# Kernel optimization log

Measured on AMD Instinct MI355X. Metric: run time of the kernel, lower is better.

Reference implementation:

```python
import jax, jax.numpy as jnp
import numpy as np

N_CAMP = 50
DAYS = 365          # execution_duration
N_STATES = 3
BASIS = 1e-10


def setup_inputs() -> dict:
    key = jax.random.key(0)
    k1, k2, k3, k4, k5 = jax.random.split(key, 5)
    adstock = jax.random.uniform(k1, (4096, N_CAMP, DAYS + 1), dtype=jnp.float32)
    mu = jax.random.normal(k2, (3,), dtype=jnp.float32)
    beta = jax.random.normal(k3, (3 * N_CAMP,), dtype=jnp.float32)
    init_prob = jax.random.normal(k4, (1,), dtype=jnp.float32)
    click_prob = jax.random.normal(k5, (1,), dtype=jnp.float32)
    return {"adstock": adstock, "mu": mu, "beta": beta,
            "init_prob": init_prob, "click_prob": click_prob}


def make_transition_matrix(mu, beta, adstock, basis=BASIS):
    b = adstock.shape[0]
    # [N_camp, 4]: zero column + reshaped betas
    beta_r = jnp.concatenate(
        [jnp.zeros((N_CAMP, 1), adstock.dtype), beta.reshape(N_CAMP, 3)], axis=1)
    # tensordot over campaign axis: [b, days, 4]
    O_beta = jnp.einsum('bcd,ck->bdk', adstock[:, :, 1:], beta_r)
    # [-inf, mu0, mu1, mu2]; exp(-inf)=0 kills the (0,0) slot exactly as in TF
    mu_full = jnp.concatenate([jnp.full((1,), -jnp.inf, dtype=mu.dtype), mu])
    mp = (mu_full[None, None, :] + O_beta).reshape(b, DAYS, N_STATES - 1, -1)
    num = jnp.exp(mp)                      # [b, D, 2, 2]
    den = 1.0 + jnp.sum(num, axis=3)       # [b, D, 2]
    main_diag = jnp.concatenate(
        [1.0 / den, jnp.ones((b, DAYS, 1), den.dtype)], axis=-1)   # [b, D, 3]
    lower_diag = jnp.concatenate(
        [num[:, :, 1:, 0] / den[:, :, 1:],
         jnp.zeros((b, DAYS, 1), den.dtype)], axis=-1)             # [b, D, 2]
    upper_diag = num[:, :, :, 1] / den                              # [b, D, 2]
    Q = jnp.zeros((b, DAYS, N_STATES, N_STATES), den.dtype)
    i = jnp.arange(N_STATES)
    Q = Q.at[..., i, i].set(main_diag)                 # main diagonal
    Q = Q.at[..., i[1:], i[:-1]].set(lower_diag)       # k = -1
    Q = Q.at[..., i[:-1], i[1:]].set(upper_diag)       # k = +1
    return jnp.maximum(Q, basis)


def reference(adstock, mu, beta, init_prob, click_prob):
    Q = make_transition_matrix(mu, beta, adstock)
    return Q, jax.nn.sigmoid(init_prob), jax.nn.sigmoid(click_prob)
```

## Files before the change

### kernel.cpp

```cpp
#include <hip/hip_runtime.h>

#define N_CAMP 50
#define DAYS   365
#define BASIS  1e-10f
#define BATCH  4096
#define NTHR   384

__global__ __launch_bounds__(NTHR)
void transition_prob_kernel(const float* __restrict__ adstock,
                            const float* __restrict__ mu,
                            const float* __restrict__ beta,
                            float* __restrict__ out)
{
    __shared__ float sb0[N_CAMP];
    __shared__ float sb1[N_CAMP];
    __shared__ float sb2[N_CAMP];
    __shared__ float smu[3];
    __shared__ float sQ[DAYS * 9];

    const int tid = threadIdx.x;
    const int b   = blockIdx.x;

    if (tid < 3 * N_CAMP) {
        const int c = tid / 3;
        const int k = tid % 3;
        const float v = beta[tid];
        if (k == 0) sb0[c] = v;
        else if (k == 1) sb1[c] = v;
        else sb2[c] = v;
    }
    if (tid < 3) smu[tid] = mu[tid];
    __syncthreads();

    const int d = tid;
    if (d < DAYS) {
        const float* arow = adstock + (size_t)b * (N_CAMP * (DAYS + 1)) + (d + 1);

        float o1 = 0.f, o2 = 0.f, o3 = 0.f;
#pragma unroll 10
        for (int c = 0; c < N_CAMP; ++c) {
            const float a = arow[(size_t)c * (DAYS + 1)];
            o1 = fmaf(a, sb0[c], o1);
            o2 = fmaf(a, sb1[c], o2);
            o3 = fmaf(a, sb2[c], o3);
        }

        const float e1 = expf(smu[0] + o1);
        const float e2 = expf(smu[1] + o2);
        const float e3 = expf(smu[2] + o3);
        const float inv0 = 1.0f / (1.0f + e1);
        const float inv1 = 1.0f / (1.0f + e2 + e3);

        float* q = &sQ[d * 9];
        q[0] = fmaxf(inv0,      BASIS);
        q[1] = fmaxf(e1 * inv0, BASIS);
        q[2] = BASIS;
        q[3] = fmaxf(e2 * inv1, BASIS);
        q[4] = fmaxf(inv1,      BASIS);
        q[5] = fmaxf(e3 * inv1, BASIS);
        q[6] = BASIS;
        q[7] = BASIS;
        q[8] = 1.0f;
    }
    __syncthreads();

    float* dst = out + (size_t)b * (DAYS * 9);
#pragma unroll
    for (int i = tid; i < DAYS * 9; i += NTHR) {
        dst[i] = sQ[i];
    }
}

__global__ void scalar_tail_kernel(const float* __restrict__ init_prob,
                                   const float* __restrict__ click_prob,
                                   float* __restrict__ out)
{
    const size_t base = (size_t)BATCH * DAYS * 9;
    if (threadIdx.x == 0) {
        out[base + 0] = 1.0f / (1.0f + expf(-init_prob[0]));
        out[base + 1] = 1.0f / (1.0f + expf(-click_prob[0]));
    }
}

extern "C" void kernel_launch(void* const* d_in, const int* in_sizes, int n_in,
                              void* d_out, int out_size, void* d_ws, size_t ws_size,
                              hipStream_t stream)
{
    const float* adstock    = (const float*)d_in[0];
    const float* mu         = (const float*)d_in[1];
    const float* beta       = (const float*)d_in[2];
    const float* init_prob  = (const float*)d_in[3];
    const float* click_prob = (const float*)d_in[4];
    float* out = (float*)d_out;

    transition_prob_kernel<<<dim3(BATCH), dim3(NTHR), 0, stream>>>(adstock, mu, beta, out);
    scalar_tail_kernel<<<1, 64, 0, stream>>>(init_prob, click_prob, out);
}
```

Baseline: 72.85 us.

## Vectorize adstock loads, process four batches per block, fuse scalar tail

Each thread now computes four consecutive days using float4 loads of adstock rows, and each block handles four batch rows with 96 threads apiece. Results are written straight to global memory, dropping the shared-memory staging buffer and its barrier. The separate sigmoid tail kernel is folded into the main kernel, removing one launch. In exchange, the float4 loads start at day offset +1 with a 366-float row stride, so they are not 16-byte aligned. The direct global stores are also strided at 36 bytes per thread rather than contiguous per block.

Measured after the change: 85.14 us. 1.17x slower.

```diff
diff --git a/kernel.cpp b/kernel.cpp
--- a/kernel.cpp
+++ b/kernel.cpp
@@ -2,24 +2,27 @@
 
 #define N_CAMP 50
 #define DAYS   365
+#define ROW    366
 #define BASIS  1e-10f
 #define BATCH  4096
-#define NTHR   384
+#define B_PER_BLK 4
+#define THR_PER_B 96
+#define NTHR   (B_PER_BLK * THR_PER_B)
 
 __global__ __launch_bounds__(NTHR)
 void transition_prob_kernel(const float* __restrict__ adstock,
                             const float* __restrict__ mu,
                             const float* __restrict__ beta,
+                            const float* __restrict__ init_prob,
+                            const float* __restrict__ click_prob,
                             float* __restrict__ out)
 {
     __shared__ float sb0[N_CAMP];
     __shared__ float sb1[N_CAMP];
     __shared__ float sb2[N_CAMP];
     __shared__ float smu[3];
-    __shared__ float sQ[DAYS * 9];
 
     const int tid = threadIdx.x;
-    const int b   = blockIdx.x;
 
     if (tid < 3 * N_CAMP) {
         const int c = tid / 3;
@@ -32,53 +35,87 @@
     if (tid < 3) smu[tid] = mu[tid];
     __syncthreads();
 
-    const int d = tid;
-    if (d < DAYS) {
-        const float* arow = adstock + (size_t)b * (N_CAMP * (DAYS + 1)) + (d + 1);
+    const int bb = tid / THR_PER_B;
+    const int q  = tid % THR_PER_B;
+    const int b  = blockIdx.x * B_PER_BLK + bb;
 
+    if (blockIdx.x == 0 && tid == THR_PER_B - 1) {
+        const size_t base = (size_t)BATCH * DAYS * 9;
+        out[base + 0] = 1.0f / (1.0f + expf(-init_prob[0]));
+        out[base + 1] = 1.0f / (1.0f + expf(-click_prob[0]));
+    }
+
+    const float m0 = smu[0], m1 = smu[1], m2 = smu[2];
+
+    if (q < 91) {
+        const float* arow = adstock + (size_t)b * (N_CAMP * ROW) + (4 * q + 1);
+
+        float o1x = 0.f, o1y = 0.f, o1z = 0.f, o1w = 0.f;
+        float o2x = 0.f, o2y = 0.f, o2z = 0.f, o2w = 0.f;
+        float o3x = 0.f, o3y = 0.f, o3z = 0.f, o3w = 0.f;
+
+#pragma unroll 10
+        for (int c = 0; c < N_CAMP; ++c) {
+            const float4 a = *reinterpret_cast<const float4*>(arow + (size_t)c * ROW);
+            const float b0 = sb0[c], b1 = sb1[c], b2 = sb2[c];
+            o1x = fmaf(a.x, b0, o1x); o1y = fmaf(a.y, b0, o1y);
+            o1z = fmaf(a.z, b0, o1z); o1w = fmaf(a.w, b0, o1w);
+            o2x = fmaf(a.x, b1, o2x); o2y = fmaf(a.y, b1, o2y);
+            o2z = fmaf(a.z, b1, o2z); o2w = fmaf(a.w, b1, o2w);
+            o3x = fmaf(a.x, b2, o3x); o3y = fmaf(a.y, b2, o3y);
+            o3z = fmaf(a.z, b2, o3z); o3w = fmaf(a.w, b2, o3w);
+        }
+
+        const float O1[4] = {o1x, o1y, o1z, o1w};
+        const float O2[4] = {o2x, o2y, o2z, o2w};
+        const float O3[4] = {o3x, o3y, o3z, o3w};
+
+#pragma unroll
+        for (int j = 0; j < 4; ++j) {
+            const int d = 4 * q + j;
+            const float e1 = expf(m0 + O1[j]);
+            const float e2 = expf(m1 + O2[j]);
+            const float e3 = expf(m2 + O3[j]);
+            const float inv0 = 1.0f / (1.0f + e1);
+            const float inv1 = 1.0f / (1.0f + e2 + e3);
+
+            float* qo = out + ((size_t)b * DAYS + d) * 9;
+            qo[0] = fmaxf(inv0,      BASIS);
+            qo[1] = fmaxf(e1 * inv0, BASIS);
+            qo[2] = BASIS;
+            qo[3] = fmaxf(e2 * inv1, BASIS);
+            qo[4] = fmaxf(inv1,      BASIS);
+            qo[5] = fmaxf(e3 * inv1, BASIS);
+            qo[6] = BASIS;
+            qo[7] = BASIS;
+            qo[8] = 1.0f;
+        }
+    } else if (q == 91) {
+        const float* arow = adstock + (size_t)b * (N_CAMP * ROW) + 365;
         float o1 = 0.f, o2 = 0.f, o3 = 0.f;
 #pragma unroll 10
         for (int c = 0; c < N_CAMP; ++c) {
-            const float a = arow[(size_t)c * (DAYS + 1)];
+            const float a = arow[(size_t)c * ROW];
             o1 = fmaf(a, sb0[c], o1);
             o2 = fmaf(a, sb1[c], o2);
             o3 = fmaf(a, sb2[c], o3);
         }
-
-        const float e1 = expf(smu[0] + o1);
-        const float e2 = expf(smu[1] + o2);
-        const float e3 = expf(smu[2] + o3);
+        const float e1 = expf(m0 + o1);
+        const float e2 = expf(m1 + o2);
+        const float e3 = expf(m2 + o3);
         const float inv0 = 1.0f / (1.0f + e1);
         const float inv1 = 1.0f / (1.0f + e2 + e3);
 
-        float* q = &sQ[d * 9];
-        q[0] = fmaxf(inv0,      BASIS);
-        q[1] = fmaxf(e1 * inv0, BASIS);
-        q[2] = BASIS;
-        q[3] = fmaxf(e2 * inv1, BASIS);
-        q[4] = fmaxf(inv1,      BASIS);
-        q[5] = fmaxf(e3 * inv1, BASIS);
-        q[6] = BASIS;
-        q[7] = BASIS;
-        q[8] = 1.0f;
-    }
-    __syncthreads();
-
-    float* dst = out + (size_t)b * (DAYS * 9);
-#pragma unroll
-    for (int i = tid; i < DAYS * 9; i += NTHR) {
-        dst[i] = sQ[i];
-    }
-}
-
-__global__ void scalar_tail_kernel(const float* __restrict__ init_prob,
-                                   const float* __restrict__ click_prob,
-                                   float* __restrict__ out)
-{
-    const size_t base = (size_t)BATCH * DAYS * 9;
-    if (threadIdx.x == 0) {
-        out[base + 0] = 1.0f / (1.0f + expf(-init_prob[0]));
-        out[base + 1] = 1.0f / (1.0f + expf(-click_prob[0]));
+        float* qo = out + ((size_t)b * DAYS + 364) * 9;
+        qo[0] = fmaxf(inv0,      BASIS);
+        qo[1] = fmaxf(e1 * inv0, BASIS);
+        qo[2] = BASIS;
+        qo[3] = fmaxf(e2 * inv1, BASIS);
+        qo[4] = fmaxf(inv1,      BASIS);
+        qo[5] = fmaxf(e3 * inv1, BASIS);
+        qo[6] = BASIS;
+        qo[7] = BASIS;
+        qo[8] = 1.0f;
     }
 }
 
@@ -93,6 +130,6 @@
     const float* click_prob = (const float*)d_in[4];
     float* out = (float*)d_out;
 
-    transition_prob_kernel<<<dim3(BATCH), dim3(NTHR), 0, stream>>>(adstock, mu, beta, out);
-    scalar_tail_kernel<<<1, 64, 0, stream>>>(init_prob, click_prob, out);
+    transition_prob_kernel<<<dim3(BATCH / B_PER_BLK), dim3(NTHR), 0, stream>>>(
+        adstock, mu, beta, init_prob, click_prob, out);
 }
```
